# Performance work log

Hardware: AMD Instinct MI355X
Metric: run time of the kernel (lower is better)

Reference implementation:

```python
import jax, jax.numpy as jnp
import numpy as np

PULL_MARGIN = 0.5
PUSH_MARGIN = 1.0
LOSS_WEIGHT = 1.0


def setup_inputs() -> dict:
    key = jax.random.key(0)
    k1, k2, k3 = jax.random.split(key, 3)
    B, C, H, W = 4, 1, 64, 96
    pred_emb = jax.random.normal(k1, (B, C, H, W), dtype=jnp.float32)
    gt_line_index = jax.random.randint(k2, (B, H, W), 0, 20, dtype=jnp.int32)
    gt_foreground_mask = jax.random.uniform(k3, (B, H, W)) < 0.3
    return {"pred_emb": pred_emb, "gt_line_index": gt_line_index,
            "gt_foreground_mask": gt_foreground_mask}


def _safe_norm(sq):
    # sqrt with zero (not NaN) gradient at 0, matching torch.norm subgradient
    safe = jnp.sqrt(jnp.where(sq > 0, sq, 1.0))
    return jnp.where(sq > 0, safe, 0.0)


def _per_sample(pred, gt, msk):
    # pred: [C,H,W] float, gt: [H,W] int, msk: [H,W] bool. P = H*W
    C = pred.shape[0]
    p = pred.reshape(C, -1)                      # [C,P]
    g = gt.reshape(-1)                           # [P]
    m = msk.reshape(-1).astype(pred.dtype)       # [P]
    pair = m[:, None] * m[None, :]               # [P,P] both-foreground mask
    sq = jnp.sum((p[:, :, None] - p[:, None, :]) ** 2, axis=0)  # [P,P]
    dist = _safe_norm(sq)
    same = jnp.where(g[:, None] == g[None, :], pair, 0.0)  # gt_square == 1 (incl diag)
    diffm = pair - same                                     # gt_square == 2
    n_same = jnp.sum(same)
    n_diff = jnp.sum(diffm)
    # pull: mean over same-line pairs of relu(dist - pull_margin); 0 if N == 0
    pull = jnp.sum(jnp.maximum(dist - PULL_MARGIN, 0.0) * same) / jnp.maximum(n_same, 1.0)
    # push: mean over diff-line pairs of relu(push_margin - dist); only if such pairs exist
    push_raw = jnp.sum(jnp.maximum(PUSH_MARGIN - dist, 0.0) * diffm) / jnp.maximum(n_diff, 1.0)
    push = jnp.where(n_diff > 0, push_raw, 0.0)
    return pull, push


def reference(pred_emb, gt_line_index, gt_foreground_mask):
    B = pred_emb.shape[0]
    pulls, pushes = jax.vmap(_per_sample)(pred_emb, gt_line_index, gt_foreground_mask)
    loss = (jnp.sum(pulls) + jnp.sum(pushes)) / B
    return loss * LOSS_WEIGHT
```

## Files before the change

### kernel.cpp

```cpp
#include <hip/hip_runtime.h>

#define B_FIXED 4
#define PULL_MARGIN 0.5f
#define PUSH_MARGIN 1.0f
#define BLOCK 256
#define TI 256
#define TJ 256
#define GRIDX 64


__device__ __forceinline__ int detect_mask_mode(const void* mask, int P) {
    __shared__ int s_flags[2];
    const unsigned int* mw = (const unsigned int*)mask;
    unsigned int not01 = 0, notf01 = 0;
    for (int idx = threadIdx.x; idx < P; idx += blockDim.x) {
        unsigned int w = mw[idx];
        not01  |= (w > 1u) ? 1u : 0u;
        notf01 |= (w != 0u && w != 0x3f800000u) ? 1u : 0u;
    }
    if (threadIdx.x == 0) { s_flags[0] = 0; s_flags[1] = 0; }
    __syncthreads();
    if (not01)  atomicOr(&s_flags[0], 1);
    if (notf01) atomicOr(&s_flags[1], 1);
    __syncthreads();
    int mode;
    if (!s_flags[0])      mode = 0;
    else if (!s_flags[1]) mode = 2;
    else                  mode = 1;
    return mode;
}

__device__ __forceinline__ bool read_fg(const void* mask, int mode, long idx) {
    if (mode == 0) return ((const int*)mask)[idx] != 0;
    if (mode == 1) return ((const unsigned char*)mask)[idx] != 0;
    return ((const float*)mask)[idx] != 0.0f;
}

__global__ __launch_bounds__(BLOCK)
void compact_kernel(const float* __restrict__ pred,
                    const int*   __restrict__ gt,
                    const void*  __restrict__ mask,
                    float* __restrict__ fgval, int* __restrict__ fgkey,
                    int* __restrict__ nfgI, int C, int P) {
    const int b   = blockIdx.y;
    const int tid = threadIdx.x;
    const int idx = blockIdx.x * BLOCK + tid;
    const int mode = detect_mask_mode(mask, P);

    bool fg = false;
    if (idx < P) fg = read_fg(mask, mode, (long)b * P + idx);

    const unsigned long long bal = __ballot(fg);
    const int lane = tid & 63;
    int base = 0;
    if (lane == 0) base = atomicAdd(&nfgI[b], (int)__popcll(bal));
    base = __shfl(base, 0);
    if (fg) {
        const int pos = base + __popcll(bal & ((1ull << lane) - 1ull));
        for (int c = 0; c < C; ++c)
            fgval[((long)b * C + c) * P + pos] = pred[((long)b * C + c) * P + idx];
        fgkey[(long)b * P + pos] = gt[(long)b * P + idx];
    }
}

__global__ __launch_bounds__(BLOCK)
void pair_kernel_c1(const float* __restrict__ fgval,
                    const int*   __restrict__ fgkey,
                    const int*   __restrict__ nfgI,
                    float* __restrict__ accF, int* __restrict__ nsI, int P) {
    const int b = blockIdx.y;
    const int n = nfgI[b];
    const float* val = fgval + (long)b * P;
    const int*   key = fgkey + (long)b * P;

    __shared__ __align__(16) float sval[TJ];
    __shared__ __align__(16) int   skey[TJ];
    __shared__ float sred[BLOCK / 64][2];
    __shared__ int   sredi[BLOCK / 64];

    const int tid  = threadIdx.x;
    const int nti  = (n + TI - 1) / TI;
    const int ntj  = (n + TJ - 1) / TJ;
    const int total = nti * ntj;

    float pull = 0.f, push = 0.f;
    int ns = 0;

    for (int t = blockIdx.x; t < total; t += gridDim.x) {
        const int ti = t / ntj, tj = t - ti * ntj;
        __syncthreads();
        {
            const int j = tj * TJ + tid;
            const bool v = j < n;
            sval[tid] = v ? val[j] : -1e30f;
            skey[tid] = v ? key[j] : -1;
        }
        const int  i  = ti * TI + tid;
        const bool iv = i < n;
        const float pi = iv ? val[i] : 1e30f;
        const int   ki = iv ? key[i] : -2;
        __syncthreads();

        const float4* sv4 = (const float4*)sval;
        const int4*   sk4 = (const int4*)skey;
        float p0 = 0.f, p1 = 0.f, q0 = 0.f, q1 = 0.f;
        int   c0 = 0, c1 = 0;
        #pragma unroll 2
        for (int g = 0; g < TJ / 4; ++g) {
            const float4 v = sv4[g];
            const int4   k = sk4[g];
            {
                const float d = fabsf(pi - v.x);
                const bool  s = (ki == k.x);
                p0 += s ? fmaxf(d - PULL_MARGIN, 0.f) : 0.f;
                q0 += s ? 0.f : fmaxf(PUSH_MARGIN - d, 0.f);
                c0 += s ? 1 : 0;
            }
            {
                const float d = fabsf(pi - v.y);
                const bool  s = (ki == k.y);
                p1 += s ? fmaxf(d - PULL_MARGIN, 0.f) : 0.f;
                q1 += s ? 0.f : fmaxf(PUSH_MARGIN - d, 0.f);
                c1 += s ? 1 : 0;
            }
            {
                const float d = fabsf(pi - v.z);
                const bool  s = (ki == k.z);
                p0 += s ? fmaxf(d - PULL_MARGIN, 0.f) : 0.f;
                q0 += s ? 0.f : fmaxf(PUSH_MARGIN - d, 0.f);
                c0 += s ? 1 : 0;
            }
            {
                const float d = fabsf(pi - v.w);
                const bool  s = (ki == k.w);
                p1 += s ? fmaxf(d - PULL_MARGIN, 0.f) : 0.f;
                q1 += s ? 0.f : fmaxf(PUSH_MARGIN - d, 0.f);
                c1 += s ? 1 : 0;
            }
        }
        pull += p0 + p1; push += q0 + q1; ns += c0 + c1;
    }

    #pragma unroll
    for (int off = 32; off > 0; off >>= 1) {
        pull += __shfl_down(pull, off);
        push += __shfl_down(push, off);
        ns   += __shfl_down(ns,   off);
    }
    const int wave = tid >> 6, lane = tid & 63;
    if (lane == 0) { sred[wave][0] = pull; sred[wave][1] = push; sredi[wave] = ns; }
    __syncthreads();
    if (tid == 0) {
        float tp = 0.f, tq = 0.f; int tn = 0;
        #pragma unroll
        for (int w = 0; w < BLOCK / 64; ++w) {
            tp += sred[w][0]; tq += sred[w][1]; tn += sredi[w];
        }
        atomicAdd(&accF[b * 4 + 0], tp);
        atomicAdd(&accF[b * 4 + 1], tq);
        atomicAdd(&nsI[b], tn);
    }
}

__global__ __launch_bounds__(BLOCK)
void pair_kernel_dyn(const float* __restrict__ fgval,
                     const int*   __restrict__ fgkey,
                     const int*   __restrict__ nfgI,
                     float* __restrict__ accF, int* __restrict__ nsI,
                     int P, int C) {
    extern __shared__ char smem[];
    float* sval = (float*)smem;
    int*   skey = (int*)(sval + (long)C * TJ);
    __shared__ float sred[BLOCK / 64][2];
    __shared__ int   sredi[BLOCK / 64];

    const int b = blockIdx.y;
    const int n = nfgI[b];
    const float* val = fgval + (long)b * C * P;
    const int*   key = fgkey + (long)b * P;

    const int tid  = threadIdx.x;
    const int nti  = (n + TI - 1) / TI;
    const int ntj  = (n + TJ - 1) / TJ;
    const int total = nti * ntj;

    float pull = 0.f, push = 0.f;
    int ns = 0;

    for (int t = blockIdx.x; t < total; t += gridDim.x) {
        const int ti = t / ntj, tj = t - ti * ntj;
        __syncthreads();
        {
            const int j = tj * TJ + tid;
            const bool v = j < n;
            for (int c = 0; c < C; ++c)
                sval[c * TJ + tid] = v ? val[(long)c * P + j] : -1e30f;
            skey[tid] = v ? key[j] : -1;
        }
        const int  i  = ti * TI + tid;
        const bool iv = i < n;
        const int  ki = iv ? key[i] : -2;
        __syncthreads();

        for (int jj = 0; jj < TJ; ++jj) {
            float sq = 0.f;
            for (int c = 0; c < C; ++c) {
                const float pi = iv ? val[(long)c * P + i] : 1e30f;
                const float d = pi - sval[c * TJ + jj];
                sq = fmaf(d, d, sq);
            }
            const float dist = sqrtf(sq);
            const bool  s = (ki == skey[jj]);
            pull += s ? fmaxf(dist - PULL_MARGIN, 0.f) : 0.f;
            push += s ? 0.f : fmaxf(PUSH_MARGIN - dist, 0.f);
            ns   += s ? 1 : 0;
        }
    }

    #pragma unroll
    for (int off = 32; off > 0; off >>= 1) {
        pull += __shfl_down(pull, off);
        push += __shfl_down(push, off);
        ns   += __shfl_down(ns,   off);
    }
    const int wave = tid >> 6, lane = tid & 63;
    if (lane == 0) { sred[wave][0] = pull; sred[wave][1] = push; sredi[wave] = ns; }
    __syncthreads();
    if (tid == 0) {
        float tp = 0.f, tq = 0.f; int tn = 0;
        #pragma unroll
        for (int w = 0; w < BLOCK / 64; ++w) {
            tp += sred[w][0]; tq += sred[w][1]; tn += sredi[w];
        }
        atomicAdd(&accF[b * 4 + 0], tp);
        atomicAdd(&accF[b * 4 + 1], tq);
        atomicAdd(&nsI[b], tn);
    }
}

__global__ __launch_bounds__(BLOCK)
void fallback_pair_kernel(const float* __restrict__ pred,
                          const int*   __restrict__ gt,
                          const void*  __restrict__ mask,
                          float* __restrict__ accF, int* __restrict__ nsI,
                          int* __restrict__ npI, int C, int P) {
    extern __shared__ char smem[];
    float* sval = (float*)smem;
    int*   skey = (int*)(sval + (long)C * TJ);
    __shared__ float sred[BLOCK / 64][2];
    __shared__ int   sredi[BLOCK / 64][2];

    const int b   = blockIdx.y;
    const int tid = threadIdx.x;
    const int mode = detect_mask_mode(mask, P);
    const long pixBase  = (long)b * P;
    const long predBase = (long)b * C * P;

    const int  i  = blockIdx.x * BLOCK + tid;
    int ki = -2;
    if (i < P) ki = read_fg(mask, mode, pixBase + i) ? gt[pixBase + i] : -2;
    const bool ifg = (ki >= 0);

    float pull = 0.f, push = 0.f;
    int ns = 0, np = 0;

    for (int j0 = 0; j0 < P; j0 += TJ) {
        __syncthreads();
        {
            const int j = j0 + tid;
            const bool v = j < P;
            bool fg = v ? read_fg(mask, mode, pixBase + j) : false;
            for (int c = 0; c < C; ++c)
                sval[c * TJ + tid] = v ? pred[predBase + (long)c * P + j] : -1e30f;
            skey[tid] = (v && fg) ? gt[pixBase + j] : -1;
        }
        __syncthreads();
        if (i < P) {
            for (int jj = 0; jj < TJ; ++jj) {
                float sq = 0.f;
                for (int c = 0; c < C; ++c) {
                    const float d = pred[predBase + (long)c * P + i] - sval[c * TJ + jj];
                    sq = fmaf(d, d, sq);
                }
                const float dist = sqrtf(sq);
                const int   kj = skey[jj];
                const bool  pm = ifg & (kj >= 0);
                const bool  s  = (ki == kj);
                pull += s ? fmaxf(dist - PULL_MARGIN, 0.f) : 0.f;
                push += (pm && !s) ? fmaxf(PUSH_MARGIN - dist, 0.f) : 0.f;
                ns   += s ? 1 : 0;
                np   += pm ? 1 : 0;
            }
        }
    }

    #pragma unroll
    for (int off = 32; off > 0; off >>= 1) {
        pull += __shfl_down(pull, off);
        push += __shfl_down(push, off);
        ns   += __shfl_down(ns,   off);
        np   += __shfl_down(np,   off);
    }
    const int wave = tid >> 6, lane = tid & 63;
    if (lane == 0) {
        sred[wave][0] = pull; sred[wave][1] = push;
        sredi[wave][0] = ns;  sredi[wave][1] = np;
    }
    __syncthreads();
    if (tid == 0) {
        float tp = 0.f, tq = 0.f; int tn = 0, tm = 0;
        #pragma unroll
        for (int w = 0; w < BLOCK / 64; ++w) {
            tp += sred[w][0]; tq += sred[w][1];
            tn += sredi[w][0]; tm += sredi[w][1];
        }
        atomicAdd(&accF[b * 4 + 0], tp);
        atomicAdd(&accF[b * 4 + 1], tq);
        atomicAdd(&nsI[b], tn);
        atomicAdd(&npI[b], tm);
    }
}

__global__ void finalize_kernel(const float* __restrict__ accF,
                                const int* __restrict__ nsI,
                                const int* __restrict__ nfgI,
                                const int* __restrict__ npI,
                                float* __restrict__ out, int pairMode) {
    if (threadIdx.x == 0 && blockIdx.x == 0) {
        float loss = 0.f;
        #pragma unroll
        for (int b = 0; b < B_FIXED; ++b) {
            const long ns  = nsI[b];
            long nd;
            if (pairMode) nd = (long)npI[b] - ns;
            else { const long nf = nfgI[b]; nd = nf * nf - ns; }
            const float pull = accF[b * 4 + 0] / (float)(ns > 1 ? ns : 1);
            const float push = (nd > 0) ? accF[b * 4 + 1] / (float)nd : 0.f;
            loss += pull + push;
        }
        out[0] = loss * (1.0f / (float)B_FIXED);
    }
}

extern "C" void kernel_launch(void* const* d_in, const int* in_sizes, int n_in,
                              void* d_out, int out_size, void* d_ws, size_t ws_size,
                              hipStream_t stream) {
    const float* pred = (const float*)d_in[0];
    const int*   gt   = (const int*)d_in[1];
    const void*  mask = d_in[2];
    float* out = (float*)d_out;

    const int C = in_sizes[0] / in_sizes[1];
    const int P = in_sizes[1] / B_FIXED;

    float* accF = (float*)d_ws;
    int*   nsI  = (int*)((char*)d_ws + 128);
    int*   nfgI = (int*)((char*)d_ws + 160);
    int*   npI  = (int*)((char*)d_ws + 192);
    float* fgval = (float*)((char*)d_ws + 1024);
    int*   fgkey = (int*)((char*)d_ws + 1024 + (size_t)B_FIXED * C * P * 4);

    hipMemsetAsync(d_ws, 0, 512, stream);

    const size_t need = 1024 + (size_t)B_FIXED * P * 4 * (size_t)(C + 1);
    if (ws_size >= need) {
        dim3 gA((P + BLOCK - 1) / BLOCK, B_FIXED);
        compact_kernel<<<gA, BLOCK, 0, stream>>>(pred, gt, mask, fgval, fgkey,
                                                 nfgI, C, P);
        dim3 gB(GRIDX, B_FIXED);
        if (C == 1)
            pair_kernel_c1<<<gB, BLOCK, 0, stream>>>(fgval, fgkey, nfgI,
                                                     accF, nsI, P);
        else
            pair_kernel_dyn<<<gB, BLOCK, (size_t)(C + 1) * TJ * 4, stream>>>(
                fgval, fgkey, nfgI, accF, nsI, P, C);
        finalize_kernel<<<1, 64, 0, stream>>>(accF, nsI, nfgI, npI, out, 0);
    } else {
        dim3 gF((P + BLOCK - 1) / BLOCK, B_FIXED);
        fallback_pair_kernel<<<gF, BLOCK, (size_t)(C + 1) * TJ * 4, stream>>>(
            pred, gt, mask, accF, nsI, npI, C, P);
        finalize_kernel<<<1, 64, 0, stream>>>(accF, nsI, nfgI, npI, out, 1);
    }
}
```

Baseline: 86.67 us.

## Fuse compaction and pair loss into one kernel with redundant per-block LDS compaction

Replaces the compact kernel, the global-memory foreground buffers and the atomic accumulators with a single fused kernel for the C==1, P==6144 case. Each block re-reads the whole sample, compacts the foreground pixels into LDS with ballot prefix sums, then works through its share of i-tiles by j-eighths directly from LDS. Per-block partials are written to a buffer and reduced by a small finalize kernel, which removes the memset, the atomics and one launch. The cost is that every block repeats the mask detection and compaction of the full sample, and the kernel now needs about 48KB of LDS per block.

```diff
diff --git a/kernel.cpp b/kernel.cpp
--- a/kernel.cpp
+++ b/kernel.cpp
@@ -1,34 +1,14 @@
 #include <hip/hip_runtime.h>
 
 #define B_FIXED 4
+#define P_FIX   6144
+#define BLOCK   256
+#define NCH     (P_FIX / BLOCK)
+#define GRIDX   64
+#define NJ      8
 #define PULL_MARGIN 0.5f
 #define PUSH_MARGIN 1.0f
-#define BLOCK 256
-#define TI 256
-#define TJ 256
-#define GRIDX 64
-
-
-__device__ __forceinline__ int detect_mask_mode(const void* mask, int P) {
-    __shared__ int s_flags[2];
-    const unsigned int* mw = (const unsigned int*)mask;
-    unsigned int not01 = 0, notf01 = 0;
-    for (int idx = threadIdx.x; idx < P; idx += blockDim.x) {
-        unsigned int w = mw[idx];
-        not01  |= (w > 1u) ? 1u : 0u;
-        notf01 |= (w != 0u && w != 0x3f800000u) ? 1u : 0u;
-    }
-    if (threadIdx.x == 0) { s_flags[0] = 0; s_flags[1] = 0; }
-    __syncthreads();
-    if (not01)  atomicOr(&s_flags[0], 1);
-    if (notf01) atomicOr(&s_flags[1], 1);
-    __syncthreads();
-    int mode;
-    if (!s_flags[0])      mode = 0;
-    else if (!s_flags[1]) mode = 2;
-    else                  mode = 1;
-    return mode;
-}
+
 
 __device__ __forceinline__ bool read_fg(const void* mask, int mode, long idx) {
     if (mode == 0) return ((const int*)mask)[idx] != 0;
@@ -37,76 +17,93 @@
 }
 
 __global__ __launch_bounds__(BLOCK)
-void compact_kernel(const float* __restrict__ pred,
-                    const int*   __restrict__ gt,
-                    const void*  __restrict__ mask,
-                    float* __restrict__ fgval, int* __restrict__ fgkey,
-                    int* __restrict__ nfgI, int C, int P) {
-    const int b   = blockIdx.y;
-    const int tid = threadIdx.x;
-    const int idx = blockIdx.x * BLOCK + tid;
-    const int mode = detect_mask_mode(mask, P);
-
-    bool fg = false;
-    if (idx < P) fg = read_fg(mask, mode, (long)b * P + idx);
-
-    const unsigned long long bal = __ballot(fg);
-    const int lane = tid & 63;
-    int base = 0;
-    if (lane == 0) base = atomicAdd(&nfgI[b], (int)__popcll(bal));
-    base = __shfl(base, 0);
-    if (fg) {
-        const int pos = base + __popcll(bal & ((1ull << lane) - 1ull));
-        for (int c = 0; c < C; ++c)
-            fgval[((long)b * C + c) * P + pos] = pred[((long)b * C + c) * P + idx];
-        fgkey[(long)b * P + pos] = gt[(long)b * P + idx];
-    }
-}
-
-__global__ __launch_bounds__(BLOCK)
-void pair_kernel_c1(const float* __restrict__ fgval,
-                    const int*   __restrict__ fgkey,
-                    const int*   __restrict__ nfgI,
-                    float* __restrict__ accF, int* __restrict__ nsI, int P) {
-    const int b = blockIdx.y;
-    const int n = nfgI[b];
-    const float* val = fgval + (long)b * P;
-    const int*   key = fgkey + (long)b * P;
-
-    __shared__ __align__(16) float sval[TJ];
-    __shared__ __align__(16) int   skey[TJ];
-    __shared__ float sred[BLOCK / 64][2];
-    __shared__ int   sredi[BLOCK / 64];
+void fused_c1(const float* __restrict__ pred,
+              const int*   __restrict__ gt,
+              const void*  __restrict__ mask,
+              float4*      __restrict__ partial) {
+    __shared__ __align__(16) float sval[P_FIX];
+    __shared__ __align__(16) int   skey[P_FIX];
+    __shared__ int   sflags[2];
+    __shared__ int   swavecnt[BLOCK / 64];
+    __shared__ float sredp[BLOCK / 64], sredq[BLOCK / 64];
+    __shared__ int   sredn[BLOCK / 64];
 
     const int tid  = threadIdx.x;
-    const int nti  = (n + TI - 1) / TI;
-    const int ntj  = (n + TJ - 1) / TJ;
-    const int total = nti * ntj;
-
+    const int b    = blockIdx.y;
+    const int wv   = tid >> 6, lane = tid & 63;
+
+    if (tid == 0) { sflags[0] = 0; sflags[1] = 0; }
+    __syncthreads();
+    {
+        const unsigned int* mw = (const unsigned int*)mask;
+        unsigned int a = 0, c = 0;
+        #pragma unroll
+        for (int k = 0; k < NCH; ++k) {
+            const unsigned int w = mw[k * BLOCK + tid];
+            a |= (w > 1u) ? 1u : 0u;
+            c |= (w != 0u && w != 0x3f800000u) ? 1u : 0u;
+        }
+        if (a) atomicOr(&sflags[0], 1);
+        if (c) atomicOr(&sflags[1], 1);
+    }
+    __syncthreads();
+    const int mode = (!sflags[0]) ? 0 : (!sflags[1] ? 2 : 1);
+
+    float val[NCH]; int key[NCH]; bool fg[NCH];
+    const long base = (long)b * P_FIX;
+    #pragma unroll
+    for (int k = 0; k < NCH; ++k) {
+        const int idx = k * BLOCK + tid;
+        fg[k]  = read_fg(mask, mode, base + idx);
+        val[k] = pred[base + idx];
+        key[k] = gt[base + idx];
+    }
+    int cnt = 0;
+    #pragma unroll
+    for (int k = 0; k < NCH; ++k)
+        cnt += (int)__popcll(__ballot(fg[k]));
+    if (lane == 0) swavecnt[wv] = cnt;
+    __syncthreads();
+    int waveoff = 0, n = 0;
+    #pragma unroll
+    for (int w = 0; w < BLOCK / 64; ++w) {
+        const int c = swavecnt[w];
+        n += c;
+        if (w < wv) waveoff += c;
+    }
+
+    int running = waveoff;
+    const unsigned long long lt = (1ull << lane) - 1ull;
+    #pragma unroll
+    for (int k = 0; k < NCH; ++k) {
+        const unsigned long long bal = __ballot(fg[k]);
+        const int pos = running + (int)__popcll(bal & lt);
+        if (fg[k]) { sval[pos] = val[k]; skey[pos] = key[k]; }
+        running += (int)__popcll(bal);
+    }
+    __syncthreads();
+
+    const int nti   = (n + BLOCK - 1) / BLOCK;
+    const int total = nti * NJ;
     float pull = 0.f, push = 0.f;
     int ns = 0;
 
-    for (int t = blockIdx.x; t < total; t += gridDim.x) {
-        const int ti = t / ntj, tj = t - ti * ntj;
-        __syncthreads();
-        {
-            const int j = tj * TJ + tid;
-            const bool v = j < n;
-            sval[tid] = v ? val[j] : -1e30f;
-            skey[tid] = v ? key[j] : -1;
-        }
-        const int  i  = ti * TI + tid;
+    for (int t = blockIdx.x; t < total; t += GRIDX) {
+        const int it = t / NJ, jt = t - it * NJ;
+        const int  i  = it * BLOCK + tid;
         const bool iv = i < n;
-        const float pi = iv ? val[i] : 1e30f;
-        const int   ki = iv ? key[i] : -2;
-        __syncthreads();
+        const float pi = iv ? sval[i] : 1e30f;
+        const int   ki = iv ? skey[i] : -2;
+        const int jlo = (jt == 0)      ? 0 : (int)(((long)jt * n / NJ) & ~3L);
+        const int jhi = (jt == NJ - 1) ? n : (int)(((long)(jt + 1) * n / NJ) & ~3L);
+        const int gve = jhi & ~3;
 
         const float4* sv4 = (const float4*)sval;
         const int4*   sk4 = (const int4*)skey;
         float p0 = 0.f, p1 = 0.f, q0 = 0.f, q1 = 0.f;
         int   c0 = 0, c1 = 0;
         #pragma unroll 2
-        for (int g = 0; g < TJ / 4; ++g) {
+        for (int g = (jlo >> 2); g < (gve >> 2); ++g) {
             const float4 v = sv4[g];
             const int4   k = sk4[g];
             {
@@ -138,6 +135,13 @@
                 c1 += s ? 1 : 0;
             }
         }
+        for (int j = gve; j < jhi; ++j) {
+            const float d = fabsf(pi - sval[j]);
+            const bool  s = (ki == skey[j]);
+            p0 += s ? fmaxf(d - PULL_MARGIN, 0.f) : 0.f;
+            q0 += s ? 0.f : fmaxf(PUSH_MARGIN - d, 0.f);
+            c0 += s ? 1 : 0;
+        }
         pull += p0 + p1; push += q0 + q1; ns += c0 + c1;
     }
 
@@ -147,95 +151,66 @@
         push += __shfl_down(push, off);
         ns   += __shfl_down(ns,   off);
     }
-    const int wave = tid >> 6, lane = tid & 63;
-    if (lane == 0) { sred[wave][0] = pull; sred[wave][1] = push; sredi[wave] = ns; }
+    if (lane == 0) { sredp[wv] = pull; sredq[wv] = push; sredn[wv] = ns; }
     __syncthreads();
     if (tid == 0) {
         float tp = 0.f, tq = 0.f; int tn = 0;
         #pragma unroll
         for (int w = 0; w < BLOCK / 64; ++w) {
-            tp += sred[w][0]; tq += sred[w][1]; tn += sredi[w];
-        }
-        atomicAdd(&accF[b * 4 + 0], tp);
-        atomicAdd(&accF[b * 4 + 1], tq);
-        atomicAdd(&nsI[b], tn);
-    }
-}
-
-__global__ __launch_bounds__(BLOCK)
-void pair_kernel_dyn(const float* __restrict__ fgval,
-                     const int*   __restrict__ fgkey,
-                     const int*   __restrict__ nfgI,
-                     float* __restrict__ accF, int* __restrict__ nsI,
-                     int P, int C) {
-    extern __shared__ char smem[];
-    float* sval = (float*)smem;
-    int*   skey = (int*)(sval + (long)C * TJ);
-    __shared__ float sred[BLOCK / 64][2];
-    __shared__ int   sredi[BLOCK / 64];
-
-    const int b = blockIdx.y;
-    const int n = nfgI[b];
-    const float* val = fgval + (long)b * C * P;
-    const int*   key = fgkey + (long)b * P;
-
-    const int tid  = threadIdx.x;
-    const int nti  = (n + TI - 1) / TI;
-    const int ntj  = (n + TJ - 1) / TJ;
-    const int total = nti * ntj;
-
-    float pull = 0.f, push = 0.f;
-    int ns = 0;
-
-    for (int t = blockIdx.x; t < total; t += gridDim.x) {
-        const int ti = t / ntj, tj = t - ti * ntj;
-        __syncthreads();
-        {
-            const int j = tj * TJ + tid;
-            const bool v = j < n;
-            for (int c = 0; c < C; ++c)
-                sval[c * TJ + tid] = v ? val[(long)c * P + j] : -1e30f;
-            skey[tid] = v ? key[j] : -1;
-        }
-        const int  i  = ti * TI + tid;
-        const bool iv = i < n;
-        const int  ki = iv ? key[i] : -2;
-        __syncthreads();
-
-        for (int jj = 0; jj < TJ; ++jj) {
-            float sq = 0.f;
-            for (int c = 0; c < C; ++c) {
-                const float pi = iv ? val[(long)c * P + i] : 1e30f;
-                const float d = pi - sval[c * TJ + jj];
-                sq = fmaf(d, d, sq);
-            }
-            const float dist = sqrtf(sq);
-            const bool  s = (ki == skey[jj]);
-            pull += s ? fmaxf(dist - PULL_MARGIN, 0.f) : 0.f;
-            push += s ? 0.f : fmaxf(PUSH_MARGIN - dist, 0.f);
-            ns   += s ? 1 : 0;
-        }
-    }
-
+            tp += sredp[w]; tq += sredq[w]; tn += sredn[w];
+        }
+        partial[b * GRIDX + blockIdx.x] =
+            make_float4(tp, tq, __int_as_float(tn), __int_as_float(n));
+    }
+}
+
+__global__ void finalize_fused(const float4* __restrict__ partial,
+                               float* __restrict__ out) {
+    __shared__ float sl[B_FIXED];
+    const int tid = threadIdx.x;
+    const int w = tid >> 6, lane = tid & 63;
+    const float4 p = partial[w * GRIDX + lane];
+    float pull = p.x, push = p.y;
+    int ns = __float_as_int(p.z);
+    const int n = __float_as_int(p.w);
     #pragma unroll
     for (int off = 32; off > 0; off >>= 1) {
         pull += __shfl_down(pull, off);
         push += __shfl_down(push, off);
         ns   += __shfl_down(ns,   off);
     }
-    const int wave = tid >> 6, lane = tid & 63;
-    if (lane == 0) { sred[wave][0] = pull; sred[wave][1] = push; sredi[wave] = ns; }
-    __syncthreads();
-    if (tid == 0) {
-        float tp = 0.f, tq = 0.f; int tn = 0;
-        #pragma unroll
-        for (int w = 0; w < BLOCK / 64; ++w) {
-            tp += sred[w][0]; tq += sred[w][1]; tn += sredi[w];
-        }
-        atomicAdd(&accF[b * 4 + 0], tp);
-        atomicAdd(&accF[b * 4 + 1], tq);
-        atomicAdd(&nsI[b], tn);
-    }
+    if (lane == 0) {
+        const long nd = (long)n * (long)n - (long)ns;
+        const float lp = pull / (float)(ns > 1 ? ns : 1);
+        const float lq = (nd > 0) ? push / (float)nd : 0.f;
+        sl[w] = lp + lq;
+    }
+    __syncthreads();
+    if (tid == 0)
+        out[0] = (sl[0] + sl[1] + sl[2] + sl[3]) * (1.0f / (float)B_FIXED);
+}
+
+#define TJ 256
+
+__device__ __forceinline__ int detect_mask_mode_g(const void* mask, int P) {
+    __shared__ int s_flags[2];
+    const unsigned int* mw = (const unsigned int*)mask;
+    unsigned int not01 = 0, notf01 = 0;
+    for (int idx = threadIdx.x; idx < P; idx += blockDim.x) {
+        unsigned int w = mw[idx];
+        not01  |= (w > 1u) ? 1u : 0u;
+        notf01 |= (w != 0u && w != 0x3f800000u) ? 1u : 0u;
+    }
+    if (threadIdx.x == 0) { s_flags[0] = 0; s_flags[1] = 0; }
+    __syncthreads();
+    if (not01)  atomicOr(&s_flags[0], 1);
+    if (notf01) atomicOr(&s_flags[1], 1);
+    __syncthreads();
+    int mode;
+    if (!s_flags[0])      mode = 0;
+    else if (!s_flags[1]) mode = 2;
+    else                  mode = 1;
+    return mode;
 }
 
 __global__ __launch_bounds__(BLOCK)
@@ -252,7 +227,7 @@
 
     const int b   = blockIdx.y;
     const int tid = threadIdx.x;
-    const int mode = detect_mask_mode(mask, P);
+    const int mode = detect_mask_mode_g(mask, P);
     const long pixBase  = (long)b * P;
     const long predBase = (long)b * C * P;
 
@@ -321,19 +296,16 @@
     }
 }
 
-__global__ void finalize_kernel(const float* __restrict__ accF,
-                                const int* __restrict__ nsI,
-                                const int* __restrict__ nfgI,
-                                const int* __restrict__ npI,
-                                float* __restrict__ out, int pairMode) {
+__global__ void finalize_fallback(const float* __restrict__ accF,
+                                  const int* __restrict__ nsI,
+                                  const int* __restrict__ npI,
+                                  float* __restrict__ out) {
     if (threadIdx.x == 0 && blockIdx.x == 0) {
         float loss = 0.f;
         #pragma unroll
         for (int b = 0; b < B_FIXED; ++b) {
-            const long ns  = nsI[b];
-            long nd;
-            if (pairMode) nd = (long)npI[b] - ns;
-            else { const long nf = nfgI[b]; nd = nf * nf - ns; }
+            const long ns = nsI[b];
+            const long nd = (long)npI[b] - ns;
             const float pull = accF[b * 4 + 0] / (float)(ns > 1 ? ns : 1);
             const float push = (nd > 0) ? accF[b * 4 + 1] / (float)nd : 0.f;
             loss += pull + push;
@@ -353,32 +325,19 @@
     const int C = in_sizes[0] / in_sizes[1];
     const int P = in_sizes[1] / B_FIXED;
 
-    float* accF = (float*)d_ws;
-    int*   nsI  = (int*)((char*)d_ws + 128);
-    int*   nfgI = (int*)((char*)d_ws + 160);
-    int*   npI  = (int*)((char*)d_ws + 192);
-    float* fgval = (float*)((char*)d_ws + 1024);
-    int*   fgkey = (int*)((char*)d_ws + 1024 + (size_t)B_FIXED * C * P * 4);
-
-    hipMemsetAsync(d_ws, 0, 512, stream);
-
-    const size_t need = 1024 + (size_t)B_FIXED * P * 4 * (size_t)(C + 1);
-    if (ws_size >= need) {
-        dim3 gA((P + BLOCK - 1) / BLOCK, B_FIXED);
-        compact_kernel<<<gA, BLOCK, 0, stream>>>(pred, gt, mask, fgval, fgkey,
-                                                 nfgI, C, P);
-        dim3 gB(GRIDX, B_FIXED);
-        if (C == 1)
-            pair_kernel_c1<<<gB, BLOCK, 0, stream>>>(fgval, fgkey, nfgI,
-                                                     accF, nsI, P);
-        else
-            pair_kernel_dyn<<<gB, BLOCK, (size_t)(C + 1) * TJ * 4, stream>>>(
-                fgval, fgkey, nfgI, accF, nsI, P, C);
-        finalize_kernel<<<1, 64, 0, stream>>>(accF, nsI, nfgI, npI, out, 0);
+    if (C == 1 && P == P_FIX && ws_size >= 4096) {
+        float4* partial = (float4*)d_ws;
+        dim3 grid(GRIDX, B_FIXED);
+        fused_c1<<<grid, BLOCK, 0, stream>>>(pred, gt, mask, partial);
+        finalize_fused<<<1, BLOCK, 0, stream>>>(partial, out);
     } else {
+        float* accF = (float*)((char*)d_ws + 4096);
+        int*   nsI  = (int*)((char*)d_ws + 4096 + 128);
+        int*   npI  = (int*)((char*)d_ws + 4096 + 192);
+        hipMemsetAsync((char*)d_ws + 4096, 0, 512, stream);
         dim3 gF((P + BLOCK - 1) / BLOCK, B_FIXED);
         fallback_pair_kernel<<<gF, BLOCK, (size_t)(C + 1) * TJ * 4, stream>>>(
             pred, gt, mask, accF, nsI, npI, C, P);
-        finalize_kernel<<<1, 64, 0, stream>>>(accF, nsI, nfgI, npI, out, 1);
-    }
-}
+        finalize_fallback<<<1, 64, 0, stream>>>(accF, nsI, npI, out);
+    }
+}
```

Result: faster. 74.49 us (-14.0%).
